# Performance work log

Measured on AMD Instinct MI355X. Metric: run time of the kernel, lower is better.

The kernel has to match this reference:

```python
import jax, jax.numpy as jnp
import numpy as np
from jax import lax

D = 1024
DI = 2 * D          # mamba inner dim
NS = 16             # ssm state size
DTR = D // 16       # dt rank = 64
KC = 4              # conv kernel
E = 8               # experts
DFF = 2 * D         # expert hidden
TOPK = 2


def _ln(x, g, b):
    mu = x.mean(-1, keepdims=True)
    var = ((x - mu) ** 2).mean(-1, keepdims=True)
    return (x - mu) * lax.rsqrt(var + 1e-5) * g + b


def _silu(x):
    return x * jax.nn.sigmoid(x)


def setup_inputs() -> dict:
    key = jax.random.key(0)
    ks = jax.random.split(key, 20)
    s = 0.02
    inp = {
        "x": jax.random.normal(ks[0], (2, 2048, D), jnp.float32),
        # layernorms
        "ln_mamba_g": jnp.ones((D,), jnp.float32),
        "ln_mamba_b": jnp.zeros((D,), jnp.float32),
        "ln_moe_g": jnp.ones((D,), jnp.float32),
        "ln_moe_b": jnp.zeros((D,), jnp.float32),
        # mamba params
        "in_proj_w": jax.random.normal(ks[1], (2 * DI, D), jnp.float32) * s,
        "in_proj_b": jnp.zeros((2 * DI,), jnp.float32),
        "conv_w": jax.random.normal(ks[2], (DI, KC), jnp.float32) * s,
        "conv_b": jnp.zeros((DI,), jnp.float32),
        "x_proj_w": jax.random.normal(ks[3], (DTR + 2 * NS, DI), jnp.float32) * s,
        "dt_proj_w": jax.random.normal(ks[4], (DI, DTR), jnp.float32) * s,
        "dt_proj_b": jnp.full((DI,), -4.6, jnp.float32),  # softplus -> small dt
        "A_log": jnp.log(jnp.broadcast_to(jnp.arange(1, NS + 1, dtype=jnp.float32), (DI, NS))),
        "D_skip": jnp.ones((DI,), jnp.float32),
        "out_proj_w": jax.random.normal(ks[5], (D, DI), jnp.float32) * s,
        # moe params
        "router_w": jax.random.normal(ks[6], (E, D), jnp.float32) * s,
        "w1": jax.random.normal(ks[7], (E, DFF, D), jnp.float32) * s,
        "b1": jnp.zeros((E, DFF), jnp.float32),
        "w2": jax.random.normal(ks[8], (E, D, DFF), jnp.float32) * s,
        "b2": jnp.zeros((E, D), jnp.float32),
    }
    return inp


def _mamba(x, in_proj_w, in_proj_b, conv_w, conv_b, x_proj_w,
           dt_proj_w, dt_proj_b, A_log, D_skip, out_proj_w):
    Bz, T, _ = x.shape
    xz = x @ in_proj_w.T + in_proj_b            # [B,T,2*DI]
    xi, z = xz[..., :DI], xz[..., DI:]
    # causal depthwise conv, kernel 4
    xp = jnp.pad(xi, ((0, 0), (KC - 1, 0), (0, 0)))
    xc = conv_b + sum(conv_w[:, k] * xp[:, k:k + T, :] for k in range(KC))
    xc = _silu(xc)                              # [B,T,DI]
    proj = xc @ x_proj_w.T                      # [B,T,DTR+2*NS]
    dt_r = proj[..., :DTR]
    Bm = proj[..., DTR:DTR + NS]                # [B,T,NS]
    Cm = proj[..., DTR + NS:]                   # [B,T,NS]
    dt = jax.nn.softplus(dt_r @ dt_proj_w.T + dt_proj_b)  # [B,T,DI]
    A = -jnp.exp(A_log)                         # [DI,NS]

    def step(h, inp):
        xt, dtt, Bt, Ct = inp                   # [B,DI],[B,DI],[B,NS],[B,NS]
        dA = jnp.exp(dtt[:, :, None] * A)       # [B,DI,NS]
        h = dA * h + (dtt * xt)[:, :, None] * Bt[:, None, :]
        y = jnp.einsum('bdn,bn->bd', h, Ct)
        return h, y

    h0 = jnp.zeros((Bz, DI, NS), x.dtype)
    xs = (xc.transpose(1, 0, 2), dt.transpose(1, 0, 2),
          Bm.transpose(1, 0, 2), Cm.transpose(1, 0, 2))
    _, ys = lax.scan(step, h0, xs)              # [T,B,DI]
    y = ys.transpose(1, 0, 2) + xc * D_skip
    y = y * _silu(z)
    return y @ out_proj_w.T                     # [B,T,D]


def _moe(x, router_w, w1, b1, w2, b2):
    logits = x @ router_w.T                     # [B,T,E]
    probs = jax.nn.softmax(logits, axis=-1)
    topv, topi = lax.top_k(probs, TOPK)
    topv = topv / topv.sum(-1, keepdims=True)
    w = (jax.nn.one_hot(topi, E, dtype=x.dtype) * topv[..., None]).sum(-2)  # [B,T,E]
    out = jnp.zeros_like(x)
    for e in range(E):                          # fixed small expert loop
        h1 = _silu(x @ w1[e].T + b1[e])
        ye = h1 @ w2[e].T + b2[e]
        out = out + w[..., e:e + 1] * ye
    return out, {"router_probs": probs}


def reference(x, ln_mamba_g, ln_mamba_b, ln_moe_g, ln_moe_b,
              in_proj_w, in_proj_b, conv_w, conv_b, x_proj_w,
              dt_proj_w, dt_proj_b, A_log, D_skip, out_proj_w,
              router_w, w1, b1, w2, b2):
    h_norm = _ln(x, ln_mamba_g, ln_mamba_b)
    mamba_out = _mamba(h_norm, in_proj_w, in_proj_b, conv_w, conv_b, x_proj_w,
                       dt_proj_w, dt_proj_b, A_log, D_skip, out_proj_w)
    h = x + mamba_out
    h_moe_in = _ln(h, ln_moe_g, ln_moe_b)
    moe_delta, aux = _moe(h_moe_in, router_w, w1, b1, w2, b2)
    h = h + moe_delta
    return (h, aux["router_probs"])
```

## Files before the change

kernel.cpp:

```cpp
#include <hip/hip_runtime.h>
#include <hip/hip_bf16.h>
#include <math.h>

#define NTOK   4096
#define TSEQ   2048
#define DMODEL 1024
#define DINNER 2048
#define NSTATE 16
#define DTRANK 64
#define NEXP   8
#define DFF    2048
#define NCHUNK 32
#define CLEN   64

typedef __attribute__((ext_vector_type(8))) short short8;
typedef __attribute__((ext_vector_type(4))) float f32x4;

__device__ __forceinline__ float fast_rcp(float x){ return __builtin_amdgcn_rcpf(x); }
__device__ __forceinline__ float siluf(float x){ return x * fast_rcp(1.f + __expf(-x)); }

__device__ __forceinline__ unsigned short f2bf(float x){
  unsigned int u = __float_as_uint(x);
  unsigned int r = (u + 0x7FFFu + ((u >> 16) & 1u)) >> 16;
  return (unsigned short)r;
}

__device__ __forceinline__ void split4(float4 a, unsigned short* hi, unsigned short* lo){
  float av[4] = {a.x, a.y, a.z, a.w};
  #pragma unroll
  for (int j=0;j<4;j++){
    unsigned short hu = f2bf(av[j]);
    float hf = __uint_as_float((unsigned int)hu << 16);
    hi[j] = hu;
    lo[j] = f2bf(av[j] - hf);
  }
}

__global__ void zero_kernel(int* __restrict__ p){ p[threadIdx.x] = 0; }

__global__ __launch_bounds__(256) void split_kernel(
    const float* __restrict__ in, unsigned short* __restrict__ hi,
    unsigned short* __restrict__ lo, int n)
{
  int i = (blockIdx.x*256 + threadIdx.x)*4;
  if (i >= n) return;
  float4 v = *(const float4*)(in + i);
  unsigned short ht[4], lt[4];
  split4(v, ht, lt);
  uint2 hw, lw;
  hw.x = (unsigned)ht[0] | ((unsigned)ht[1]<<16);
  hw.y = (unsigned)ht[2] | ((unsigned)ht[3]<<16);
  lw.x = (unsigned)lt[0] | ((unsigned)lt[1]<<16);
  lw.y = (unsigned)lt[2] | ((unsigned)lt[3]<<16);
  *(uint2*)(hi+i) = hw;
  *(uint2*)(lo+i) = lw;
}

template<int EPI, int BM>
__global__ __launch_bounds__(256) void gemm_mfma(
    const float* __restrict__ A, int lda,
    const unsigned short* __restrict__ Whi, const unsigned short* __restrict__ Wlo, int ldw,
    int M, int N, int K,
    const float* __restrict__ bias,
    const float* __restrict__ resid, int ldr,
    float* __restrict__ out, int ldo)
{
  constexpr int TA = BM/8;
  constexpr int RG = BM/64;
  const int tid = threadIdx.x;
  const int m0 = blockIdx.y * BM;
  const int n0 = blockIdx.x * 64;

  __shared__ __align__(16) unsigned short Ahs[BM*40];
  __shared__ __align__(16) unsigned short Als[BM*40];
  __shared__ __align__(16) unsigned short Whs[64*40];
  __shared__ __align__(16) unsigned short Wls[64*40];

  const int arow = tid / (32/TA);
  const int ak   = (tid % (32/TA)) * TA;
  const int wrow = tid >> 2;
  const int wk   = (tid & 3) * 8;

  const float* Ap = A + (size_t)(m0 + arow)*lda + ak;
  const bool wok = (n0 + wrow) < N;
  const unsigned short* Whp = Whi + (size_t)(n0 + wrow)*ldw + wk;
  const unsigned short* Wlp = Wlo + (size_t)(n0 + wrow)*ldw + wk;

  const int lane = tid & 63;
  const int wv   = tid >> 6;
  const int qd   = lane >> 4;
  const int mr   = lane & 15;

  f32x4 acc[RG][4];
  #pragma unroll
  for (int rg=0; rg<RG; rg++)
    #pragma unroll
    for (int ct=0; ct<4; ct++) acc[rg][ct] = (f32x4){0.f,0.f,0.f,0.f};

  const unsigned short* ardh = &Ahs[(wv*(16*RG) + mr)*40 + qd*8];
  const unsigned short* ardl = &Als[(wv*(16*RG) + mr)*40 + qd*8];
  const unsigned short* brdh = &Whs[mr*40 + qd*8];
  const unsigned short* brdl = &Wls[mr*40 + qd*8];

  const short8 z8 = {0,0,0,0,0,0,0,0};

  for (int kt = 0; kt < K; kt += 32){
    short8 ahi[TA/8], alo[TA/8];
    #pragma unroll
    for (int h=0; h<TA/8; h++){
      unsigned short ht[8], lt[8];
      split4(*(const float4*)(Ap + kt + h*8),     ht,   lt);
      split4(*(const float4*)(Ap + kt + h*8 + 4), ht+4, lt+4);
      #pragma unroll
      for (int j=0;j<8;j++){ ahi[h][j]=(short)ht[j]; alo[h][j]=(short)lt[j]; }
    }
    short8 wh8 = wok ? *(const short8*)(Whp + kt) : z8;
    short8 wl8 = wok ? *(const short8*)(Wlp + kt) : z8;
    __syncthreads();
    #pragma unroll
    for (int h=0; h<TA/8; h++){
      *(short8*)&Ahs[arow*40 + ak + h*8] = ahi[h];
      *(short8*)&Als[arow*40 + ak + h*8] = alo[h];
    }
    *(short8*)&Whs[wrow*40 + wk] = wh8;
    *(short8*)&Wls[wrow*40 + wk] = wl8;
    __syncthreads();
    #pragma unroll
    for (int rg=0; rg<RG; rg++){
      short8 ah = *(const short8*)(ardh + rg*16*40);
      short8 al = *(const short8*)(ardl + rg*16*40);
      #pragma unroll
      for (int ct=0; ct<4; ct++){
        short8 bh = *(const short8*)(brdh + ct*16*40);
        short8 bl = *(const short8*)(brdl + ct*16*40);
        f32x4 t = acc[rg][ct];
        t = __builtin_amdgcn_mfma_f32_16x16x32_bf16(ah, bh, t, 0,0,0);
        t = __builtin_amdgcn_mfma_f32_16x16x32_bf16(al, bh, t, 0,0,0);
        t = __builtin_amdgcn_mfma_f32_16x16x32_bf16(ah, bl, t, 0,0,0);
        acc[rg][ct] = t;
      }
    }
  }

  #pragma unroll
  for (int rg=0; rg<RG; rg++){
    #pragma unroll
    for (int ct=0; ct<4; ct++){
      int colg = n0 + ct*16 + mr;
      if (colg >= N) continue;
      float bias_v = (EPI==0 || EPI==2) ? bias[colg] : 0.f;
      #pragma unroll
      for (int r=0;r<4;r++){
        int rowg = m0 + wv*(16*RG) + rg*16 + qd*4 + r;
        float v = acc[rg][ct][r];
        if (EPI == 0){ v += bias_v; }
        else if (EPI == 2){ v += bias_v; v = (v > 20.f) ? v : log1pf(expf(v)); }
        else if (EPI == 3){ v += resid[(size_t)rowg*ldr + colg]; }
        out[(size_t)rowg*ldo + colg] = v;
      }
    }
  }
}

__global__ __launch_bounds__(256) void ln_kernel(
    const float* __restrict__ x, const float* __restrict__ g, const float* __restrict__ b,
    float* __restrict__ out)
{
  int tok = blockIdx.x;
  int tid = threadIdx.x;
  const float* row = x + (size_t)tok * DMODEL;
  float v[4];
  float s = 0.f, sq = 0.f;
  #pragma unroll
  for (int j=0;j<4;j++){
    v[j] = row[j*256 + tid];
    s += v[j]; sq += v[j]*v[j];
  }
  #pragma unroll
  for (int o=1;o<64;o<<=1){ s += __shfl_xor(s,o,64); sq += __shfl_xor(sq,o,64); }
  __shared__ float ss[4], ssq[4];
  int wid = tid >> 6, lane = tid & 63;
  if (lane == 0){ ss[wid]=s; ssq[wid]=sq; }
  __syncthreads();
  s  = ss[0]+ss[1]+ss[2]+ss[3];
  sq = ssq[0]+ssq[1]+ssq[2]+ssq[3];
  float mu = s * (1.f/DMODEL);
  float var = sq * (1.f/DMODEL) - mu*mu;
  float rs = rsqrtf(var + 1e-5f);
  #pragma unroll
  for (int j=0;j<4;j++){
    int d = j*256 + tid;
    out[(size_t)tok*DMODEL + d] = (v[j]-mu)*rs*g[d] + b[d];
  }
}

__global__ __launch_bounds__(256) void conv_kernel(
    const float* __restrict__ xz, const float* __restrict__ cw,
    const float* __restrict__ cb, float* __restrict__ xc)
{
  int i = blockIdx.x*256 + threadIdx.x;
  int tok = i >> 11;
  int ch  = i & 2047;
  int t   = tok & (TSEQ-1);
  int b   = tok >> 11;
  float acc = cb[ch];
  #pragma unroll
  for (int k=0;k<4;k++){
    int tt = t + k - 3;
    if (tt >= 0)
      acc = fmaf(cw[ch*4 + k], xz[(size_t)((b<<11)+tt)*4096 + ch], acc);
  }
  xc[i] = siluf(acc);
}

__global__ __launch_bounds__(256) void scan_partial(
    const float* __restrict__ xz, const float* __restrict__ xc,
    const float* __restrict__ proj, const float* __restrict__ A_log,
    float* __restrict__ P, float* __restrict__ Q)
{
  int tid = threadIdx.x;
  int ch  = blockIdx.x*256 + tid;
  int c   = blockIdx.y;
  int b   = blockIdx.z;
  float A[16];
  #pragma unroll
  for (int n=0;n<16;n++) A[n] = -expf(A_log[ch*NSTATE + n]);
  float h[16];
  #pragma unroll
  for (int n=0;n<16;n++) h[n] = 0.f;
  float sdt = 0.f;
  int tok0 = (b<<11) + c*CLEN;
  float dtv = xz[(size_t)tok0*4096 + ch];
  float xt  = xc[(size_t)tok0*2048 + ch];
  for (int i=0;i<CLEN;i++){
    int tn = tok0 + ((i+1 < CLEN) ? i+1 : i);
    float dtv_n = xz[(size_t)tn*4096 + ch];
    float xt_n  = xc[(size_t)tn*2048 + ch];
    const float4* pB = (const float4*)(proj + (size_t)(tok0+i)*96 + 64);
    float Bv[16];
    *(float4*)&Bv[0]  = pB[0];
    *(float4*)&Bv[4]  = pB[1];
    *(float4*)&Bv[8]  = pB[2];
    *(float4*)&Bv[12] = pB[3];
    float dxt = dtv*xt;
    sdt += dtv;
    #pragma unroll
    for (int n=0;n<16;n++){
      float dA = __expf(dtv*A[n]);
      h[n] = fmaf(dA, h[n], dxt*Bv[n]);
    }
    dtv = dtv_n; xt = xt_n;
  }
  size_t base = ((((size_t)(b*NCHUNK + c))<<11 | ch)<<4);
  #pragma unroll
  for (int n=0;n<16;n++){
    P[base+n] = __expf(A[n]*sdt);
    Q[base+n] = h[n];
  }
}

__global__ __launch_bounds__(256) void scan_combine(
    const float* __restrict__ Q, float* PH)
{
  int g = blockIdx.x*256 + threadIdx.x;
  int n = g & 15, ch = (g>>4) & 2047, b = g>>15;
  float hs = 0.f;
  for (int c=0;c<NCHUNK;c++){
    size_t idx = ((((size_t)(b*NCHUNK + c))<<11 | ch)<<4) | n;
    float pv = PH[idx];
    float qv = Q[idx];
    PH[idx] = hs;
    hs = fmaf(pv, hs, qv);
  }
}

__global__ __launch_bounds__(256) void scan_final(
    const float* __restrict__ xz, float* __restrict__ xc,
    const float* __restrict__ proj, const float* __restrict__ A_log,
    const float* __restrict__ Dskip, const float* __restrict__ Hs)
{
  int tid = threadIdx.x;
  int ch  = blockIdx.x*256 + tid;
  int c   = blockIdx.y;
  int b   = blockIdx.z;
  float A[16];
  #pragma unroll
  for (int n=0;n<16;n++) A[n] = -expf(A_log[ch*NSTATE + n]);
  float Dv = Dskip[ch];
  size_t base = ((((size_t)(b*NCHUNK + c))<<11 | ch)<<4);
  float h[16];
  #pragma unroll
  for (int n=0;n<16;n++) h[n] = Hs[base+n];
  int tok0 = (b<<11) + c*CLEN;
  float dtv = xz[(size_t)tok0*4096 + ch];
  float xt  = xc[(size_t)tok0*2048 + ch];
  float zv  = xz[(size_t)tok0*4096 + 2048 + ch];
  for (int i=0;i<CLEN;i++){
    int tn = tok0 + ((i+1 < CLEN) ? i+1 : i);
    float dtv_n = xz[(size_t)tn*4096 + ch];
    float xt_n  = xc[(size_t)tn*2048 + ch];
    float zv_n  = xz[(size_t)tn*4096 + 2048 + ch];
    const float4* pB = (const float4*)(proj + (size_t)(tok0+i)*96 + 64);
    float Bv[16], Cv[16];
    *(float4*)&Bv[0]  = pB[0];
    *(float4*)&Bv[4]  = pB[1];
    *(float4*)&Bv[8]  = pB[2];
    *(float4*)&Bv[12] = pB[3];
    *(float4*)&Cv[0]  = pB[4];
    *(float4*)&Cv[4]  = pB[5];
    *(float4*)&Cv[8]  = pB[6];
    *(float4*)&Cv[12] = pB[7];
    float dxt = dtv*xt;
    float y = xt*Dv;
    #pragma unroll
    for (int n=0;n<16;n++){
      float dA = __expf(dtv*A[n]);
      h[n] = fmaf(dA, h[n], dxt*Bv[n]);
      y = fmaf(h[n], Cv[n], y);
    }
    xc[(size_t)(tok0+i)*2048 + ch] = y * siluf(zv);
    dtv = dtv_n; xt = xt_n; zv = zv_n;
  }
}

__global__ __launch_bounds__(256) void router_kernel(
    const float* __restrict__ hmoe, const float* __restrict__ rw,
    float* __restrict__ probs_out, int* __restrict__ cnt,
    int* __restrict__ tok_e0, int* __restrict__ tok_e1,
    float* __restrict__ tok_w0, float* __restrict__ tok_w1)
{
  int tok = blockIdx.x;
  int tid = threadIdx.x;
  int e = tid >> 5, l = tid & 31;
  float s = 0.f;
  const float* row = hmoe + (size_t)tok*DMODEL;
  const float* wr  = rw + (size_t)e*DMODEL;
  for (int d=l; d<DMODEL; d+=32) s = fmaf(row[d], wr[d], s);
  #pragma unroll
  for (int o=1;o<32;o<<=1) s += __shfl_xor(s,o,64);
  __shared__ float lg[8];
  if (l==0) lg[e]=s;
  __syncthreads();
  if (tid==0){
    float mx = lg[0];
    for (int k=1;k<8;k++) mx = fmaxf(mx, lg[k]);
    float pe[8]; float den=0.f;
    for (int k=0;k<8;k++){ pe[k]=expf(lg[k]-mx); den+=pe[k]; }
    float inv = 1.f/den;
    for (int k=0;k<8;k++) probs_out[tok*8+k] = pe[k]*inv;
    int i0=0;
    for (int k=1;k<8;k++) if (pe[k] > pe[i0]) i0=k;
    int i1 = (i0==0)?1:0;
    for (int k=0;k<8;k++) if (k!=i0 && pe[k] > pe[i1]) i1=k;
    float v0=pe[i0], v1=pe[i1], sw=v0+v1;
    tok_e0[tok]=i0; tok_e1[tok]=i1;
    tok_w0[tok]=v0/sw; tok_w1[tok]=v1/sw;
    atomicAdd(&cnt[i0],1); atomicAdd(&cnt[i1],1);
  }
}

__global__ void prefix_kernel(const int* cnt, int* off, int* fill){
  if (threadIdx.x==0){
    int s=0;
    for (int e=0;e<NEXP;e++){ off[e]=s; s+=cnt[e]; fill[e]=0; }
  }
}

__global__ __launch_bounds__(256) void fill_kernel(
    const int* tok_e0, const int* tok_e1, const float* tok_w0, const float* tok_w1,
    const int* off, int* fill, int* slot_tok, float* slot_w)
{
  int tok = blockIdx.x*256 + threadIdx.x;
  int e0=tok_e0[tok], e1=tok_e1[tok];
  int p0 = atomicAdd(&fill[e0],1); int s0 = off[e0]+p0;
  slot_tok[s0]=tok; slot_w[s0]=tok_w0[tok];
  int p1 = atomicAdd(&fill[e1],1); int s1 = off[e1]+p1;
  slot_tok[s1]=tok; slot_w[s1]=tok_w1[tok];
}

__global__ __launch_bounds__(256) void moe_gemm1(
    const float* __restrict__ hmoe, const float* __restrict__ w1, const float* __restrict__ b1,
    const int* __restrict__ cnt, const int* __restrict__ off,
    const int* __restrict__ slot_tok, unsigned short* __restrict__ H1)
{
  int e = blockIdx.z;
  int c = cnt[e];
  int r0 = blockIdx.y*64;
  if (r0 >= c) return;
  int base = off[e];
  int tid = threadIdx.x;
  __shared__ int toks[64];
  if (tid < 64) toks[tid] = (r0 + tid < c) ? slot_tok[base + r0 + tid] : -1;
  __shared__ __align__(16) unsigned short As[64*40];
  __shared__ __align__(16) unsigned short Ws[64*40];
  __syncthreads();

  const int n0   = blockIdx.x*64;
  const int arow = tid >> 2;
  const int kq   = (tid & 3) * 8;
  const int tok  = toks[arow];
  const float* Ap = hmoe + (size_t)(tok < 0 ? 0 : tok)*DMODEL + kq;
  const bool aok  = (tok >= 0);
  const float* Wp = w1 + (size_t)e*DFF*DMODEL + (size_t)(n0+arow)*DMODEL + kq;

  const int lane = tid & 63;
  const int wv   = tid >> 6;
  const int qd   = lane >> 4;
  const int mr   = lane & 15;

  f32x4 acc0={0,0,0,0}, acc1={0,0,0,0}, acc2={0,0,0,0}, acc3={0,0,0,0};

  unsigned short* aw = &As[arow*40 + kq];
  unsigned short* ww = &Ws[arow*40 + kq];
  const unsigned short* ard = &As[(wv*16 + mr)*40 + qd*8];
  const unsigned short* brd = &Ws[mr*40 + qd*8];

  for (int kt = 0; kt < DMODEL; kt += 32){
    float4 a0 = aok ? *(const float4*)(Ap + kt)     : make_float4(0,0,0,0);
    float4 a1 = aok ? *(const float4*)(Ap + kt + 4) : make_float4(0,0,0,0);
    float4 w0 = *(const float4*)(Wp + kt);
    float4 w1v= *(const float4*)(Wp + kt + 4);
    short8 av, wvv;
    av[0]=(short)f2bf(a0.x); av[1]=(short)f2bf(a0.y); av[2]=(short)f2bf(a0.z); av[3]=(short)f2bf(a0.w);
    av[4]=(short)f2bf(a1.x); av[5]=(short)f2bf(a1.y); av[6]=(short)f2bf(a1.z); av[7]=(short)f2bf(a1.w);
    wvv[0]=(short)f2bf(w0.x); wvv[1]=(short)f2bf(w0.y); wvv[2]=(short)f2bf(w0.z); wvv[3]=(short)f2bf(w0.w);
    wvv[4]=(short)f2bf(w1v.x); wvv[5]=(short)f2bf(w1v.y); wvv[6]=(short)f2bf(w1v.z); wvv[7]=(short)f2bf(w1v.w);
    __syncthreads();
    *(short8*)aw = av;
    *(short8*)ww = wvv;
    __syncthreads();
    short8 af = *(const short8*)ard;
    short8 b0 = *(const short8*)(brd);
    short8 b1f= *(const short8*)(brd + 16*40);
    short8 b2f= *(const short8*)(brd + 32*40);
    short8 b3f= *(const short8*)(brd + 48*40);
    acc0 = __builtin_amdgcn_mfma_f32_16x16x32_bf16(af, b0, acc0, 0,0,0);
    acc1 = __builtin_amdgcn_mfma_f32_16x16x32_bf16(af, b1f, acc1, 0,0,0);
    acc2 = __builtin_amdgcn_mfma_f32_16x16x32_bf16(af, b2f, acc2, 0,0,0);
    acc3 = __builtin_amdgcn_mfma_f32_16x16x32_bf16(af, b3f, acc3, 0,0,0);
  }

  #pragma unroll
  for (int ct=0; ct<4; ct++){
    f32x4 a = (ct==0)?acc0:(ct==1)?acc1:(ct==2)?acc2:acc3;
    int colg = n0 + ct*16 + mr;
    float bias = b1[(size_t)e*DFF + colg];
    #pragma unroll
    for (int r=0;r<4;r++){
      int sl = wv*16 + qd*4 + r;
      if (toks[sl] < 0) continue;
      float v = a[r] + bias;
      H1[(size_t)(base + r0 + sl)*DFF + colg] = f2bf(siluf(v));
    }
  }
}

__global__ __launch_bounds__(256) void moe_gemm2(
    const unsigned short* __restrict__ H1, const float* __restrict__ w2,
    const float* __restrict__ b2,
    const int* __restrict__ cnt, const int* __restrict__ off,
    const int* __restrict__ slot_tok, const float* __restrict__ slot_w,
    float* __restrict__ hres)
{
  int e = blockIdx.z;
  int c = cnt[e];
  int r0 = blockIdx.y*64;
  if (r0 >= c) return;
  int base = off[e];
  int tid = threadIdx.x;
  __shared__ int toks[64];
  __shared__ float wts[64];
  if (tid < 64){
    int r = r0 + tid;
    toks[tid] = (r<c) ? slot_tok[base+r] : -1;
    wts[tid]  = (r<c) ? slot_w[base+r] : 0.f;
  }
  __shared__ __align__(16) unsigned short As[64*40];
  __shared__ __align__(16) unsigned short Ws[64*40];
  __syncthreads();

  const int n0   = blockIdx.x*64;
  const int arow = tid >> 2;
  const int kq   = (tid & 3) * 8;
  const bool aok = (toks[arow] >= 0);
  const unsigned short* Ap = H1 + (size_t)(base + r0 + (aok ? arow : 0))*DFF + kq;
  const float* Wp = w2 + (size_t)e*DMODEL*DFF + (size_t)(n0+arow)*DFF + kq;

  const int lane = tid & 63;
  const int wv   = tid >> 6;
  const int qd   = lane >> 4;
  const int mr   = lane & 15;

  f32x4 acc0={0,0,0,0}, acc1={0,0,0,0}, acc2={0,0,0,0}, acc3={0,0,0,0};

  unsigned short* aw = &As[arow*40 + kq];
  unsigned short* ww = &Ws[arow*40 + kq];
  const unsigned short* ard = &As[(wv*16 + mr)*40 + qd*8];
  const unsigned short* brd = &Ws[mr*40 + qd*8];

  const short8 zero8 = {0,0,0,0,0,0,0,0};
  for (int kt = 0; kt < DFF; kt += 32){
    short8 av = aok ? *(const short8*)(Ap + kt) : zero8;
    float4 w0 = *(const float4*)(Wp + kt);
    float4 w1v= *(const float4*)(Wp + kt + 4);
    short8 wvv;
    wvv[0]=(short)f2bf(w0.x); wvv[1]=(short)f2bf(w0.y); wvv[2]=(short)f2bf(w0.z); wvv[3]=(short)f2bf(w0.w);
    wvv[4]=(short)f2bf(w1v.x); wvv[5]=(short)f2bf(w1v.y); wvv[6]=(short)f2bf(w1v.z); wvv[7]=(short)f2bf(w1v.w);
    __syncthreads();
    *(short8*)aw = av;
    *(short8*)ww = wvv;
    __syncthreads();
    short8 af = *(const short8*)ard;
    short8 b0 = *(const short8*)(brd);
    short8 b1f= *(const short8*)(brd + 16*40);
    short8 b2f= *(const short8*)(brd + 32*40);
    short8 b3f= *(const short8*)(brd + 48*40);
    acc0 = __builtin_amdgcn_mfma_f32_16x16x32_bf16(af, b0, acc0, 0,0,0);
    acc1 = __builtin_amdgcn_mfma_f32_16x16x32_bf16(af, b1f, acc1, 0,0,0);
    acc2 = __builtin_amdgcn_mfma_f32_16x16x32_bf16(af, b2f, acc2, 0,0,0);
    acc3 = __builtin_amdgcn_mfma_f32_16x16x32_bf16(af, b3f, acc3, 0,0,0);
  }

  #pragma unroll
  for (int ct=0; ct<4; ct++){
    f32x4 a = (ct==0)?acc0:(ct==1)?acc1:(ct==2)?acc2:acc3;
    int colg = n0 + ct*16 + mr;
    float bias = b2[(size_t)e*DMODEL + colg];
    #pragma unroll
    for (int r=0;r<4;r++){
      int sl = wv*16 + qd*4 + r;
      int t = toks[sl];
      if (t < 0) continue;
      float v = a[r] + bias;
      atomicAdd(&hres[(size_t)t*DMODEL + colg], wts[sl]*v);
    }
  }
}

__global__ __launch_bounds__(256) void final_kernel(const float* __restrict__ hres,
                                                    float* __restrict__ out)
{
  int i = blockIdx.x*256 + threadIdx.x;
  out[i] = hres[i];
}

extern "C" void kernel_launch(void* const* d_in, const int* in_sizes, int n_in,
                              void* d_out, int out_size, void* d_ws, size_t ws_size,
                              hipStream_t stream)
{
  const float* x         = (const float*)d_in[0];
  const float* ln_m_g    = (const float*)d_in[1];
  const float* ln_m_b    = (const float*)d_in[2];
  const float* ln_e_g    = (const float*)d_in[3];
  const float* ln_e_b    = (const float*)d_in[4];
  const float* in_proj_w = (const float*)d_in[5];
  const float* in_proj_b = (const float*)d_in[6];
  const float* conv_w    = (const float*)d_in[7];
  const float* conv_b    = (const float*)d_in[8];
  const float* x_proj_w  = (const float*)d_in[9];
  const float* dt_proj_w = (const float*)d_in[10];
  const float* dt_proj_b = (const float*)d_in[11];
  const float* A_log     = (const float*)d_in[12];
  const float* D_skip    = (const float*)d_in[13];
  const float* out_proj_w= (const float*)d_in[14];
  const float* router_w  = (const float*)d_in[15];
  const float* w1        = (const float*)d_in[16];
  const float* b1        = (const float*)d_in[17];
  const float* w2        = (const float*)d_in[18];
  const float* b2        = (const float*)d_in[19];

  char* ws = (char*)d_ws;
  float* xz   = (float*)(ws + 0);
  float* xc   = (float*)(ws + 67108864ull);
  float* proj = (float*)(ws + 100663296ull);
  char*  misc = ws + 102236160ull;
  float* hres = (float*)(ws + 0);
  unsigned short* H1 = (unsigned short*)(ws + 16777216ull);
  float* hn   = (float*)d_out;
  float* Pbuf = (float*)d_out;
  float* Qbuf = (float*)d_out + (2u<<20);

  unsigned short* Wi_hi = (unsigned short*)(ws + 67108864ull);
  unsigned short* Wi_lo = Wi_hi + 4194304;
  unsigned short* Wo_hi = (unsigned short*)(ws + 33554432ull);
  unsigned short* Wo_lo = Wo_hi + 2097152;
  unsigned short* Wx_hi = (unsigned short*)d_out;
  unsigned short* Wx_lo = Wx_hi + 196608;
  unsigned short* Wd_hi = Wx_lo + 196608;
  unsigned short* Wd_lo = Wd_hi + 131072;

  int*   cnt      = (int*)(misc);
  int*   fill     = (int*)(misc + 64);
  int*   offp     = (int*)(misc + 128);
  int*   tok_e0   = (int*)(misc + 1024);
  int*   tok_e1   = (int*)(misc + 1024 + 16384);
  float* tok_w0   = (float*)(misc + 1024 + 32768);
  float* tok_w1   = (float*)(misc + 1024 + 49152);
  int*   slot_tok = (int*)(misc + 1024 + 65536);
  float* slot_w   = (float*)(misc + 1024 + 98304);
  float* out_h    = (float*)d_out;
  float* probs_out= (float*)d_out + 4194304;

  zero_kernel<<<1, 64, 0, stream>>>(cnt);

  split_kernel<<<4096, 256, 0, stream>>>(in_proj_w, Wi_hi, Wi_lo, 4194304);
  ln_kernel<<<NTOK, 256, 0, stream>>>(x, ln_m_g, ln_m_b, hn);
  gemm_mfma<0,128><<<dim3(64, 32), 256, 0, stream>>>(
      hn, DMODEL, Wi_hi, Wi_lo, DMODEL, NTOK, 4096, DMODEL,
      in_proj_b, nullptr, 0, xz, 4096);
  split_kernel<<<192, 256, 0, stream>>>(x_proj_w, Wx_hi, Wx_lo, 196608);
  split_kernel<<<128, 256, 0, stream>>>(dt_proj_w, Wd_hi, Wd_lo, 131072);
  conv_kernel<<<NTOK*DINNER/256, 256, 0, stream>>>(xz, conv_w, conv_b, xc);
  gemm_mfma<1,64><<<dim3(2, 64), 256, 0, stream>>>(
      xc, DINNER, Wx_hi, Wx_lo, DINNER, NTOK, 96, DINNER,
      nullptr, nullptr, 0, proj, 96);
  gemm_mfma<2,128><<<dim3(32, 32), 256, 0, stream>>>(
      proj, 96, Wd_hi, Wd_lo, DTRANK, NTOK, DINNER, DTRANK,
      dt_proj_b, nullptr, 0, xz, 4096);
  scan_partial<<<dim3(DINNER/256, NCHUNK, 2), 256, 0, stream>>>(
      xz, xc, proj, A_log, Pbuf, Qbuf);
  scan_combine<<<256, 256, 0, stream>>>(Qbuf, Pbuf);
  scan_final<<<dim3(DINNER/256, NCHUNK, 2), 256, 0, stream>>>(
      xz, xc, proj, A_log, D_skip, Pbuf);
  split_kernel<<<2048, 256, 0, stream>>>(out_proj_w, Wo_hi, Wo_lo, 2097152);
  gemm_mfma<3,128><<<dim3(16, 32), 256, 0, stream>>>(
      xc, DINNER, Wo_hi, Wo_lo, DINNER, NTOK, DMODEL, DINNER,
      nullptr, x, DMODEL, hres, DMODEL);

  ln_kernel<<<NTOK, 256, 0, stream>>>(hres, ln_e_g, ln_e_b, hn);
  router_kernel<<<NTOK, 256, 0, stream>>>(hn, router_w, probs_out, cnt,
                                          tok_e0, tok_e1, tok_w0, tok_w1);
  prefix_kernel<<<1, 64, 0, stream>>>(cnt, offp, fill);
  fill_kernel<<<NTOK/256, 256, 0, stream>>>(tok_e0, tok_e1, tok_w0, tok_w1,
                                            offp, fill, slot_tok, slot_w);
  moe_gemm1<<<dim3(DFF/64, 64, NEXP), 256, 0, stream>>>(
      hn, w1, b1, cnt, offp, slot_tok, H1);
  moe_gemm2<<<dim3(DMODEL/64, 64, NEXP), 256, 0, stream>>>(
      H1, w2, b2, cnt, offp, slot_tok, slot_w, hres);

  final_kernel<<<NTOK*DMODEL/256, 256, 0, stream>>>(hres, out_h);
}
```

Measured before the change: 1.091 ms.

## Enlarge GEMM tiles to 128 columns and pre-convert MoE weights and activations to bf16

Mamba GEMMs now use 128-column weight tiles, and the in_proj GEMM reads pre-split hi/lo bf16 activations that the first layernorm writes directly. The MoE GEMMs move from 64x64 to 128x128 tiles, and w1/w2 are converted to bf16 in one pass each before their GEMMs, so the inner loops no longer convert fp32 per tile. The goal is more MFMA work per shared-memory load and less repeated conversion work. The cost is larger register and LDS use per block, fewer blocks for the skinny GEMMs, and an extra full read and write of the expert weights.

```diff
diff --git a/kernel.cpp b/kernel.cpp
--- a/kernel.cpp
+++ b/kernel.cpp
@@ -56,46 +56,63 @@
   *(uint2*)(lo+i) = lw;
 }
 
-template<int EPI, int BM>
-__global__ __launch_bounds__(256) void gemm_mfma(
-    const float* __restrict__ A, int lda,
+__global__ __launch_bounds__(256) void cvt_bf_kernel(
+    const float* __restrict__ in, unsigned short* __restrict__ out, int n)
+{
+  int i = (blockIdx.x*256 + threadIdx.x)*8;
+  if (i >= n) return;
+  float4 a = *(const float4*)(in+i);
+  float4 b = *(const float4*)(in+i+4);
+  short8 v;
+  v[0]=(short)f2bf(a.x); v[1]=(short)f2bf(a.y); v[2]=(short)f2bf(a.z); v[3]=(short)f2bf(a.w);
+  v[4]=(short)f2bf(b.x); v[5]=(short)f2bf(b.y); v[6]=(short)f2bf(b.z); v[7]=(short)f2bf(b.w);
+  *(short8*)(out+i) = v;
+}
+
+template<int EPI, int BM, bool PS>
+__global__ __launch_bounds__(256) void gemm_big(
+    const float* __restrict__ A,
+    const unsigned short* __restrict__ Ahi, const unsigned short* __restrict__ Alo, int lda,
     const unsigned short* __restrict__ Whi, const unsigned short* __restrict__ Wlo, int ldw,
     int M, int N, int K,
     const float* __restrict__ bias,
     const float* __restrict__ resid, int ldr,
     float* __restrict__ out, int ldo)
 {
-  constexpr int TA = BM/8;
-  constexpr int RG = BM/64;
+  constexpr int RG  = BM/64;
+  constexpr int TPR = 256/BM;
+  constexpr int EA  = 32/TPR;
   const int tid = threadIdx.x;
   const int m0 = blockIdx.y * BM;
-  const int n0 = blockIdx.x * 64;
+  const int n0 = blockIdx.x * 128;
 
   __shared__ __align__(16) unsigned short Ahs[BM*40];
   __shared__ __align__(16) unsigned short Als[BM*40];
-  __shared__ __align__(16) unsigned short Whs[64*40];
-  __shared__ __align__(16) unsigned short Wls[64*40];
-
-  const int arow = tid / (32/TA);
-  const int ak   = (tid % (32/TA)) * TA;
-  const int wrow = tid >> 2;
-  const int wk   = (tid & 3) * 8;
-
-  const float* Ap = A + (size_t)(m0 + arow)*lda + ak;
+  __shared__ __align__(16) unsigned short Whs[128*40];
+  __shared__ __align__(16) unsigned short Wls[128*40];
+
+  const int arow = tid / TPR;
+  const int aseg = (tid % TPR) * EA;
+  const int wrow = tid >> 1;
+  const int wseg = (tid & 1) * 16;
+
+  const float* Ap = PS ? nullptr : (A + (size_t)(m0 + arow)*lda + aseg);
+  const unsigned short* Aph = PS ? (Ahi + (size_t)(m0 + arow)*lda + aseg) : nullptr;
+  const unsigned short* Apl = PS ? (Alo + (size_t)(m0 + arow)*lda + aseg) : nullptr;
   const bool wok = (n0 + wrow) < N;
-  const unsigned short* Whp = Whi + (size_t)(n0 + wrow)*ldw + wk;
-  const unsigned short* Wlp = Wlo + (size_t)(n0 + wrow)*ldw + wk;
+  const unsigned short* Whp = Whi + (size_t)(n0 + wrow)*ldw + wseg;
+  const unsigned short* Wlp = Wlo + (size_t)(n0 + wrow)*ldw + wseg;
 
   const int lane = tid & 63;
   const int wv   = tid >> 6;
   const int qd   = lane >> 4;
   const int mr   = lane & 15;
 
-  f32x4 acc[RG][4];
+  f32x4 acc[RG][8];
   #pragma unroll
   for (int rg=0; rg<RG; rg++)
     #pragma unroll
-    for (int ct=0; ct<4; ct++) acc[rg][ct] = (f32x4){0.f,0.f,0.f,0.f};
+    for (int ct=0; ct<8; ct++) acc[rg][ct] = (f32x4){0.f,0.f,0.f,0.f};
 
   const unsigned short* ardh = &Ahs[(wv*(16*RG) + mr)*40 + qd*8];
   const unsigned short* ardl = &Als[(wv*(16*RG) + mr)*40 + qd*8];
@@ -105,38 +122,53 @@
   const short8 z8 = {0,0,0,0,0,0,0,0};
 
   for (int kt = 0; kt < K; kt += 32){
-    short8 ahi[TA/8], alo[TA/8];
-    #pragma unroll
-    for (int h=0; h<TA/8; h++){
-      unsigned short ht[8], lt[8];
-      split4(*(const float4*)(Ap + kt + h*8),     ht,   lt);
-      split4(*(const float4*)(Ap + kt + h*8 + 4), ht+4, lt+4);
+    short8 ah[EA/8], al[EA/8];
+    if (PS){
       #pragma unroll
-      for (int j=0;j<8;j++){ ahi[h][j]=(short)ht[j]; alo[h][j]=(short)lt[j]; }
-    }
-    short8 wh8 = wok ? *(const short8*)(Whp + kt) : z8;
-    short8 wl8 = wok ? *(const short8*)(Wlp + kt) : z8;
+      for (int h=0; h<EA/8; h++){
+        ah[h] = *(const short8*)(Aph + kt + h*8);
+        al[h] = *(const short8*)(Apl + kt + h*8);
+      }
+    } else {
+      #pragma unroll
+      for (int q=0; q<EA/4; q++){
+        float4 f = *(const float4*)(Ap + kt + q*4);
+        unsigned short ht[4], lt[4];
+        split4(f, ht, lt);
+        #pragma unroll
+        for (int j=0;j<4;j++){
+          ah[(q*4+j)/8][(q*4+j)&7] = (short)ht[j];
+          al[(q*4+j)/8][(q*4+j)&7] = (short)lt[j];
+        }
+      }
+    }
+    short8 wh0 = wok ? *(const short8*)(Whp + kt)     : z8;
+    short8 wh1 = wok ? *(const short8*)(Whp + kt + 8) : z8;
+    short8 wl0 = wok ? *(const short8*)(Wlp + kt)     : z8;
+    short8 wl1 = wok ? *(const short8*)(Wlp + kt + 8) : z8;
     __syncthreads();
     #pragma unroll
-    for (int h=0; h<TA/8; h++){
-      *(short8*)&Ahs[arow*40 + ak + h*8] = ahi[h];
-      *(short8*)&Als[arow*40 + ak + h*8] = alo[h];
-    }
-    *(short8*)&Whs[wrow*40 + wk] = wh8;
-    *(short8*)&Wls[wrow*40 + wk] = wl8;
+    for (int h=0; h<EA/8; h++){
+      *(short8*)&Ahs[arow*40 + aseg + h*8] = ah[h];
+      *(short8*)&Als[arow*40 + aseg + h*8] = al[h];
+    }
+    *(short8*)&Whs[wrow*40 + wseg]     = wh0;
+    *(short8*)&Whs[wrow*40 + wseg + 8] = wh1;
+    *(short8*)&Wls[wrow*40 + wseg]     = wl0;
+    *(short8*)&Wls[wrow*40 + wseg + 8] = wl1;
     __syncthreads();
     #pragma unroll
     for (int rg=0; rg<RG; rg++){
-      short8 ah = *(const short8*)(ardh + rg*16*40);
-      short8 al = *(const short8*)(ardl + rg*16*40);
+      short8 af = *(const short8*)(ardh + rg*16*40);
+      short8 alf= *(const short8*)(ardl + rg*16*40);
       #pragma unroll
-      for (int ct=0; ct<4; ct++){
+      for (int ct=0; ct<8; ct++){
         short8 bh = *(const short8*)(brdh + ct*16*40);
         short8 bl = *(const short8*)(brdl + ct*16*40);
         f32x4 t = acc[rg][ct];
-        t = __builtin_amdgcn_mfma_f32_16x16x32_bf16(ah, bh, t, 0,0,0);
-        t = __builtin_amdgcn_mfma_f32_16x16x32_bf16(al, bh, t, 0,0,0);
-        t = __builtin_amdgcn_mfma_f32_16x16x32_bf16(ah, bl, t, 0,0,0);
+        t = __builtin_amdgcn_mfma_f32_16x16x32_bf16(af, bh, t, 0,0,0);
+        t = __builtin_amdgcn_mfma_f32_16x16x32_bf16(alf, bh, t, 0,0,0);
+        t = __builtin_amdgcn_mfma_f32_16x16x32_bf16(af, bl, t, 0,0,0);
         acc[rg][ct] = t;
       }
     }
@@ -145,7 +177,7 @@
   #pragma unroll
   for (int rg=0; rg<RG; rg++){
     #pragma unroll
-    for (int ct=0; ct<4; ct++){
+    for (int ct=0; ct<8; ct++){
       int colg = n0 + ct*16 + mr;
       if (colg >= N) continue;
       float bias_v = (EPI==0 || EPI==2) ? bias[colg] : 0.f;
@@ -162,9 +194,9 @@
   }
 }
 
-__global__ __launch_bounds__(256) void ln_kernel(
+__global__ __launch_bounds__(256) void ln_split_kernel(
     const float* __restrict__ x, const float* __restrict__ g, const float* __restrict__ b,
-    float* __restrict__ out)
+    unsigned short* __restrict__ hi, unsigned short* __restrict__ lo)
 {
   int tok = blockIdx.x;
   int tid = threadIdx.x;
@@ -190,7 +222,45 @@
   #pragma unroll
   for (int j=0;j<4;j++){
     int d = j*256 + tid;
-    out[(size_t)tok*DMODEL + d] = (v[j]-mu)*rs*g[d] + b[d];
+    float o = (v[j]-mu)*rs*g[d] + b[d];
+    unsigned short hu = f2bf(o);
+    float hf = __uint_as_float((unsigned int)hu << 16);
+    hi[(size_t)tok*DMODEL + d] = hu;
+    lo[(size_t)tok*DMODEL + d] = f2bf(o - hf);
+  }
+}
+
+__global__ __launch_bounds__(256) void ln2_kernel(
+    const float* __restrict__ x, const float* __restrict__ g, const float* __restrict__ b,
+    float* __restrict__ out, unsigned short* __restrict__ outb)
+{
+  int tok = blockIdx.x;
+  int tid = threadIdx.x;
+  const float* row = x + (size_t)tok * DMODEL;
+  float v[4];
+  float s = 0.f, sq = 0.f;
+  #pragma unroll
+  for (int j=0;j<4;j++){
+    v[j] = row[j*256 + tid];
+    s += v[j]; sq += v[j]*v[j];
+  }
+  #pragma unroll
+  for (int o=1;o<64;o<<=1){ s += __shfl_xor(s,o,64); sq += __shfl_xor(sq,o,64); }
+  __shared__ float ss[4], ssq[4];
+  int wid = tid >> 6, lane = tid & 63;
+  if (lane == 0){ ss[wid]=s; ssq[wid]=sq; }
+  __syncthreads();
+  s  = ss[0]+ss[1]+ss[2]+ss[3];
+  sq = ssq[0]+ssq[1]+ssq[2]+ssq[3];
+  float mu = s * (1.f/DMODEL);
+  float var = sq * (1.f/DMODEL) - mu*mu;
+  float rs = rsqrtf(var + 1e-5f);
+  #pragma unroll
+  for (int j=0;j<4;j++){
+    int d = j*256 + tid;
+    float o = (v[j]-mu)*rs*g[d] + b[d];
+    out[(size_t)tok*DMODEL + d] = o;
+    outb[(size_t)tok*DMODEL + d] = f2bf(o);
   }
 }
 
@@ -379,84 +449,87 @@
 }
 
 __global__ __launch_bounds__(256) void moe_gemm1(
-    const float* __restrict__ hmoe, const float* __restrict__ w1, const float* __restrict__ b1,
+    const unsigned short* __restrict__ hnb, const unsigned short* __restrict__ w1b,
+    const float* __restrict__ b1,
     const int* __restrict__ cnt, const int* __restrict__ off,
     const int* __restrict__ slot_tok, unsigned short* __restrict__ H1)
 {
   int e = blockIdx.z;
   int c = cnt[e];
-  int r0 = blockIdx.y*64;
+  int r0 = blockIdx.y*128;
   if (r0 >= c) return;
   int base = off[e];
   int tid = threadIdx.x;
-  __shared__ int toks[64];
-  if (tid < 64) toks[tid] = (r0 + tid < c) ? slot_tok[base + r0 + tid] : -1;
-  __shared__ __align__(16) unsigned short As[64*40];
-  __shared__ __align__(16) unsigned short Ws[64*40];
+  __shared__ int toks[128];
+  if (tid < 128) toks[tid] = (r0 + tid < c) ? slot_tok[base + r0 + tid] : -1;
+  __shared__ __align__(16) unsigned short As[128*40];
+  __shared__ __align__(16) unsigned short Ws[128*40];
   __syncthreads();
 
-  const int n0   = blockIdx.x*64;
-  const int arow = tid >> 2;
-  const int kq   = (tid & 3) * 8;
-  const int tok  = toks[arow];
-  const float* Ap = hmoe + (size_t)(tok < 0 ? 0 : tok)*DMODEL + kq;
-  const bool aok  = (tok >= 0);
-  const float* Wp = w1 + (size_t)e*DFF*DMODEL + (size_t)(n0+arow)*DMODEL + kq;
+  const int n0   = blockIdx.x*128;
+  const int srow = tid >> 1;
+  const int sseg = (tid & 1) * 16;
+  const int tok  = toks[srow];
+  const bool aok = (tok >= 0);
+  const unsigned short* Ap = hnb + (size_t)(aok ? tok : 0)*DMODEL + sseg;
+  const unsigned short* Wp = w1b + (size_t)e*DFF*DMODEL + (size_t)(n0+srow)*DMODEL + sseg;
 
   const int lane = tid & 63;
   const int wv   = tid >> 6;
   const int qd   = lane >> 4;
   const int mr   = lane & 15;
 
-  f32x4 acc0={0,0,0,0}, acc1={0,0,0,0}, acc2={0,0,0,0}, acc3={0,0,0,0};
-
-  unsigned short* aw = &As[arow*40 + kq];
-  unsigned short* ww = &Ws[arow*40 + kq];
-  const unsigned short* ard = &As[(wv*16 + mr)*40 + qd*8];
+  f32x4 acc[2][8];
+  #pragma unroll
+  for (int rg=0; rg<2; rg++)
+    #pragma unroll
+    for (int ct=0; ct<8; ct++) acc[rg][ct] = (f32x4){0.f,0.f,0.f,0.f};
+
+  const unsigned short* ard = &As[(wv*32 + mr)*40 + qd*8];
   const unsigned short* brd = &Ws[mr*40 + qd*8];
+  const short8 z8 = {0,0,0,0,0,0,0,0};
 
   for (int kt = 0; kt < DMODEL; kt += 32){
-    float4 a0 = aok ? *(const float4*)(Ap + kt)     : make_float4(0,0,0,0);
-    float4 a1 = aok ? *(const float4*)(Ap + kt + 4) : make_float4(0,0,0,0);
-    float4 w0 = *(const float4*)(Wp + kt);
-    float4 w1v= *(const float4*)(Wp + kt + 4);
-    short8 av, wvv;
-    av[0]=(short)f2bf(a0.x); av[1]=(short)f2bf(a0.y); av[2]=(short)f2bf(a0.z); av[3]=(short)f2bf(a0.w);
-    av[4]=(short)f2bf(a1.x); av[5]=(short)f2bf(a1.y); av[6]=(short)f2bf(a1.z); av[7]=(short)f2bf(a1.w);
-    wvv[0]=(short)f2bf(w0.x); wvv[1]=(short)f2bf(w0.y); wvv[2]=(short)f2bf(w0.z); wvv[3]=(short)f2bf(w0.w);
-    wvv[4]=(short)f2bf(w1v.x); wvv[5]=(short)f2bf(w1v.y); wvv[6]=(short)f2bf(w1v.z); wvv[7]=(short)f2bf(w1v.w);
+    short8 a0 = aok ? *(const short8*)(Ap + kt)     : z8;
+    short8 a1 = aok ? *(const short8*)(Ap + kt + 8) : z8;
+    short8 w0 = *(const short8*)(Wp + kt);
+    short8 w1v= *(const short8*)(Wp + kt + 8);
     __syncthreads();
-    *(short8*)aw = av;
-    *(short8*)ww = wvv;
+    *(short8*)&As[srow*40 + sseg]     = a0;
+    *(short8*)&As[srow*40 + sseg + 8] = a1;
+    *(short8*)&Ws[srow*40 + sseg]     = w0;
+    *(short8*)&Ws[srow*40 + sseg + 8] = w1v;
     __syncthreads();
-    short8 af = *(const short8*)ard;
-    short8 b0 = *(const short8*)(brd);
-    short8 b1f= *(const short8*)(brd + 16*40);
-    short8 b2f= *(const short8*)(brd + 32*40);
-    short8 b3f= *(const short8*)(brd + 48*40);
-    acc0 = __builtin_amdgcn_mfma_f32_16x16x32_bf16(af, b0, acc0, 0,0,0);
-    acc1 = __builtin_amdgcn_mfma_f32_16x16x32_bf16(af, b1f, acc1, 0,0,0);
-    acc2 = __builtin_amdgcn_mfma_f32_16x16x32_bf16(af, b2f, acc2, 0,0,0);
-    acc3 = __builtin_amdgcn_mfma_f32_16x16x32_bf16(af, b3f, acc3, 0,0,0);
-  }
-
-  #pragma unroll
-  for (int ct=0; ct<4; ct++){
-    f32x4 a = (ct==0)?acc0:(ct==1)?acc1:(ct==2)?acc2:acc3;
-    int colg = n0 + ct*16 + mr;
-    float bias = b1[(size_t)e*DFF + colg];
-    #pragma unroll
-    for (int r=0;r<4;r++){
-      int sl = wv*16 + qd*4 + r;
-      if (toks[sl] < 0) continue;
-      float v = a[r] + bias;
-      H1[(size_t)(base + r0 + sl)*DFF + colg] = f2bf(siluf(v));
+    #pragma unroll
+    for (int rg=0; rg<2; rg++){
+      short8 af = *(const short8*)(ard + rg*16*40);
+      #pragma unroll
+      for (int ct=0; ct<8; ct++){
+        short8 bf = *(const short8*)(brd + ct*16*40);
+        acc[rg][ct] = __builtin_amdgcn_mfma_f32_16x16x32_bf16(af, bf, acc[rg][ct], 0,0,0);
+      }
+    }
+  }
+
+  #pragma unroll
+  for (int rg=0; rg<2; rg++){
+    #pragma unroll
+    for (int ct=0; ct<8; ct++){
+      int colg = n0 + ct*16 + mr;
+      float bias = b1[(size_t)e*DFF + colg];
+      #pragma unroll
+      for (int r=0;r<4;r++){
+        int sl = wv*32 + rg*16 + qd*4 + r;
+        if (toks[sl] < 0) continue;
+        float v = acc[rg][ct][r] + bias;
+        H1[(size_t)(base + r0 + sl)*DFF + colg] = f2bf(siluf(v));
+      }
     }
   }
 }
 
 __global__ __launch_bounds__(256) void moe_gemm2(
-    const unsigned short* __restrict__ H1, const float* __restrict__ w2,
+    const unsigned short* __restrict__ H1, const unsigned short* __restrict__ w2b,
     const float* __restrict__ b2,
     const int* __restrict__ cnt, const int* __restrict__ off,
     const int* __restrict__ slot_tok, const float* __restrict__ slot_w,
@@ -464,75 +537,79 @@
 {
   int e = blockIdx.z;
   int c = cnt[e];
-  int r0 = blockIdx.y*64;
+  int r0 = blockIdx.y*128;
   if (r0 >= c) return;
   int base = off[e];
   int tid = threadIdx.x;
-  __shared__ int toks[64];
-  __shared__ float wts[64];
-  if (tid < 64){
+  __shared__ int toks[128];
+  __shared__ float wts[128];
+  if (tid < 128){
     int r = r0 + tid;
     toks[tid] = (r<c) ? slot_tok[base+r] : -1;
     wts[tid]  = (r<c) ? slot_w[base+r] : 0.f;
   }
-  __shared__ __align__(16) unsigned short As[64*40];
-  __shared__ __align__(16) unsigned short Ws[64*40];
+  __shared__ __align__(16) unsigned short As[128*40];
+  __shared__ __align__(16) unsigned short Ws[128*40];
   __syncthreads();
 
-  const int n0   = blockIdx.x*64;
-  const int arow = tid >> 2;
-  const int kq   = (tid & 3) * 8;
-  const bool aok = (toks[arow] >= 0);
-  const unsigned short* Ap = H1 + (size_t)(base + r0 + (aok ? arow : 0))*DFF + kq;
-  const float* Wp = w2 + (size_t)e*DMODEL*DFF + (size_t)(n0+arow)*DFF + kq;
+  const int n0   = blockIdx.x*128;
+  const int srow = tid >> 1;
+  const int sseg = (tid & 1) * 16;
+  const bool aok = (toks[srow] >= 0);
+  const unsigned short* Ap = H1 + (size_t)(base + r0 + (aok ? srow : 0))*DFF + sseg;
+  const unsigned short* Wp = w2b + (size_t)e*DMODEL*DFF + (size_t)(n0+srow)*DFF + sseg;
 
   const int lane = tid & 63;
   const int wv   = tid >> 6;
   const int qd   = lane >> 4;
   const int mr   = lane & 15;
 
-  f32x4 acc0={0,0,0,0}, acc1={0,0,0,0}, acc2={0,0,0,0}, acc3={0,0,0,0};
-
-  unsigned short* aw = &As[arow*40 + kq];
-  unsigned short* ww = &Ws[arow*40 + kq];
-  const unsigned short* ard = &As[(wv*16 + mr)*40 + qd*8];
+  f32x4 acc[2][8];
+  #pragma unroll
+  for (int rg=0; rg<2; rg++)
+    #pragma unroll
+    for (int ct=0; ct<8; ct++) acc[rg][ct] = (f32x4){0.f,0.f,0.f,0.f};
+
+  const unsigned short* ard = &As[(wv*32 + mr)*40 + qd*8];
   const unsigned short* brd = &Ws[mr*40 + qd*8];
-
-  const short8 zero8 = {0,0,0,0,0,0,0,0};
+  const short8 z8 = {0,0,0,0,0,0,0,0};
+
   for (int kt = 0; kt < DFF; kt += 32){
-    short8 av = aok ? *(const short8*)(Ap + kt) : zero8;
-    float4 w0 = *(const float4*)(Wp + kt);
-    float4 w1v= *(const float4*)(Wp + kt + 4);
-    short8 wvv;
-    wvv[0]=(short)f2bf(w0.x); wvv[1]=(short)f2bf(w0.y); wvv[2]=(short)f2bf(w0.z); wvv[3]=(short)f2bf(w0.w);
-    wvv[4]=(short)f2bf(w1v.x); wvv[5]=(short)f2bf(w1v.y); wvv[6]=(short)f2bf(w1v.z); wvv[7]=(short)f2bf(w1v.w);
+    short8 a0 = aok ? *(const short8*)(Ap + kt)     : z8;
+    short8 a1 = aok ? *(const short8*)(Ap + kt + 8) : z8;
+    short8 w0 = *(const short8*)(Wp + kt);
+    short8 w1v= *(const short8*)(Wp + kt + 8);
     __syncthreads();
-    *(short8*)aw = av;
-    *(short8*)ww = wvv;
+    *(short8*)&As[srow*40 + sseg]     = a0;
+    *(short8*)&As[srow*40 + sseg + 8] = a1;
+    *(short8*)&Ws[srow*40 + sseg]     = w0;
+    *(short8*)&Ws[srow*40 + sseg + 8] = w1v;
     __syncthreads();
-    short8 af = *(const short8*)ard;
-    short8 b0 = *(const short8*)(brd);
-    short8 b1f= *(const short8*)(brd + 16*40);
-    short8 b2f= *(const short8*)(brd + 32*40);
-    short8 b3f= *(const short8*)(brd + 48*40);
-    acc0 = __builtin_amdgcn_mfma_f32_16x16x32_bf16(af, b0, acc0, 0,0,0);
-    acc1 = __builtin_amdgcn_mfma_f32_16x16x32_bf16(af, b1f, acc1, 0,0,0);
-    acc2 = __builtin_amdgcn_mfma_f32_16x16x32_bf16(af, b2f, acc2, 0,0,0);
-    acc3 = __builtin_amdgcn_mfma_f32_16x16x32_bf16(af, b3f, acc3, 0,0,0);
-  }
-
-  #pragma unroll
-  for (int ct=0; ct<4; ct++){
-    f32x4 a = (ct==0)?acc0:(ct==1)?acc1:(ct==2)?acc2:acc3;
-    int colg = n0 + ct*16 + mr;
-    float bias = b2[(size_t)e*DMODEL + colg];
-    #pragma unroll
-    for (int r=0;r<4;r++){
-      int sl = wv*16 + qd*4 + r;
-      int t = toks[sl];
-      if (t < 0) continue;
-      float v = a[r] + bias;
-      atomicAdd(&hres[(size_t)t*DMODEL + colg], wts[sl]*v);
+    #pragma unroll
+    for (int rg=0; rg<2; rg++){
+      short8 af = *(const short8*)(ard + rg*16*40);
+      #pragma unroll
+      for (int ct=0; ct<8; ct++){
+        short8 bf = *(const short8*)(brd + ct*16*40);
+        acc[rg][ct] = __builtin_amdgcn_mfma_f32_16x16x32_bf16(af, bf, acc[rg][ct], 0,0,0);
+      }
+    }
+  }
+
+  #pragma unroll
+  for (int rg=0; rg<2; rg++){
+    #pragma unroll
+    for (int ct=0; ct<8; ct++){
+      int colg = n0 + ct*16 + mr;
+      float bias = b2[(size_t)e*DMODEL + colg];
+      #pragma unroll
+      for (int r=0;r<4;r++){
+        int sl = wv*32 + rg*16 + qd*4 + r;
+        int t = toks[sl];
+        if (t < 0) continue;
+        float v = acc[rg][ct][r] + bias;
+        atomicAdd(&hres[(size_t)t*DMODEL + colg], wts[sl]*v);
+      }
     }
   }
 }
@@ -575,7 +652,12 @@
   float* proj = (float*)(ws + 100663296ull);
   char*  misc = ws + 102236160ull;
   float* hres = (float*)(ws + 0);
-  unsigned short* H1 = (unsigned short*)(ws + 16777216ull);
+  unsigned short* H1    = (unsigned short*)(ws + 16777216ull);
+  unsigned short* hn_bf = (unsigned short*)(ws + 50331648ull);
+  unsigned short* wmoe  = (unsigned short*)(ws + 67108864ull);
+
+  unsigned short* hn_hi = (unsigned short*)d_out;
+  unsigned short* hn_lo = hn_hi + 4194304;
   float* hn   = (float*)d_out;
   float* Pbuf = (float*)d_out;
   float* Qbuf = (float*)d_out + (2u<<20);
@@ -604,18 +686,18 @@
   zero_kernel<<<1, 64, 0, stream>>>(cnt);
 
   split_kernel<<<4096, 256, 0, stream>>>(in_proj_w, Wi_hi, Wi_lo, 4194304);
-  ln_kernel<<<NTOK, 256, 0, stream>>>(x, ln_m_g, ln_m_b, hn);
-  gemm_mfma<0,128><<<dim3(64, 32), 256, 0, stream>>>(
-      hn, DMODEL, Wi_hi, Wi_lo, DMODEL, NTOK, 4096, DMODEL,
+  ln_split_kernel<<<NTOK, 256, 0, stream>>>(x, ln_m_g, ln_m_b, hn_hi, hn_lo);
+  gemm_big<0,128,true><<<dim3(32, 32), 256, 0, stream>>>(
+      nullptr, hn_hi, hn_lo, DMODEL, Wi_hi, Wi_lo, DMODEL, NTOK, 4096, DMODEL,
       in_proj_b, nullptr, 0, xz, 4096);
   split_kernel<<<192, 256, 0, stream>>>(x_proj_w, Wx_hi, Wx_lo, 196608);
   split_kernel<<<128, 256, 0, stream>>>(dt_proj_w, Wd_hi, Wd_lo, 131072);
   conv_kernel<<<NTOK*DINNER/256, 256, 0, stream>>>(xz, conv_w, conv_b, xc);
-  gemm_mfma<1,64><<<dim3(2, 64), 256, 0, stream>>>(
-      xc, DINNER, Wx_hi, Wx_lo, DINNER, NTOK, 96, DINNER,
+  gemm_big<1,64,false><<<dim3(1, 64), 256, 0, stream>>>(
+      xc, nullptr, nullptr, DINNER, Wx_hi, Wx_lo, DINNER, NTOK, 96, DINNER,
       nullptr, nullptr, 0, proj, 96);
-  gemm_mfma<2,128><<<dim3(32, 32), 256, 0, stream>>>(
-      proj, 96, Wd_hi, Wd_lo, DTRANK, NTOK, DINNER, DTRANK,
+  gemm_big<2,128,false><<<dim3(16, 32), 256, 0, stream>>>(
+      proj, nullptr, nullptr, 96, Wd_hi, Wd_lo, DTRANK, NTOK, DINNER, DTRANK,
       dt_proj_b, nullptr, 0, xz, 4096);
   scan_partial<<<dim3(DINNER/256, NCHUNK, 2), 256, 0, stream>>>(
       xz, xc, proj, A_log, Pbuf, Qbuf);
@@ -623,20 +705,22 @@
   scan_final<<<dim3(DINNER/256, NCHUNK, 2), 256, 0, stream>>>(
       xz, xc, proj, A_log, D_skip, Pbuf);
   split_kernel<<<2048, 256, 0, stream>>>(out_proj_w, Wo_hi, Wo_lo, 2097152);
-  gemm_mfma<3,128><<<dim3(16, 32), 256, 0, stream>>>(
-      xc, DINNER, Wo_hi, Wo_lo, DINNER, NTOK, DMODEL, DINNER,
+  gemm_big<3,128,false><<<dim3(8, 32), 256, 0, stream>>>(
+      xc, nullptr, nullptr, DINNER, Wo_hi, Wo_lo, DINNER, NTOK, DMODEL, DINNER,
       nullptr, x, DMODEL, hres, DMODEL);
 
-  ln_kernel<<<NTOK, 256, 0, stream>>>(hres, ln_e_g, ln_e_b, hn);
+  ln2_kernel<<<NTOK, 256, 0, stream>>>(hres, ln_e_g, ln_e_b, hn, hn_bf);
   router_kernel<<<NTOK, 256, 0, stream>>>(hn, router_w, probs_out, cnt,
                                           tok_e0, tok_e1, tok_w0, tok_w1);
   prefix_kernel<<<1, 64, 0, stream>>>(cnt, offp, fill);
   fill_kernel<<<NTOK/256, 256, 0, stream>>>(tok_e0, tok_e1, tok_w0, tok_w1,
                                             offp, fill, slot_tok, slot_w);
-  moe_gemm1<<<dim3(DFF/64, 64, NEXP), 256, 0, stream>>>(
-      hn, w1, b1, cnt, offp, slot_tok, H1);
-  moe_gemm2<<<dim3(DMODEL/64, 64, NEXP), 256, 0, stream>>>(
-      H1, w2, b2, cnt, offp, slot_tok, slot_w, hres);
+  cvt_bf_kernel<<<8192, 256, 0, stream>>>(w1, wmoe, NEXP*DFF*DMODEL);
+  moe_gemm1<<<dim3(DFF/128, 32, NEXP), 256, 0, stream>>>(
+      hn_bf, wmoe, b1, cnt, offp, slot_tok, H1);
+  cvt_bf_kernel<<<8192, 256, 0, stream>>>(w2, wmoe, NEXP*DMODEL*DFF);
+  moe_gemm2<<<dim3(DMODEL/128, 32, NEXP), 256, 0, stream>>>(
+      H1, wmoe, b2, cnt, offp, slot_tok, slot_w, hres);
 
   final_kernel<<<NTOK*DMODEL/256, 256, 0, stream>>>(hres, out_h);
 }
```

Measured after the change: 1.056 ms. 1.03x faster.
